# Optimization experiments

Hardware: AMD Instinct MI355X
Metric: run time of the kernel (lower is better)

Reference implementation:

```python
import jax, jax.numpy as jnp
import numpy as np

HID = 2048; H = 16; QLR = 1536; KVLR = 512
DN = 128   # qk_nope_head_dim
DR = 64    # qk_rope_head_dim
DV = 128   # v_head_dim
EPS = 1e-6
B, S = 2, 2048


def rmsnorm(x):
    return x * jax.lax.rsqrt(jnp.mean(x * x, axis=-1, keepdims=True) + EPS)


def rope_tables(seq_len):
    inv_freq = 1.0 / (10000.0 ** (jnp.arange(0, DR, 2, dtype=jnp.float32) / DR))  # [DR/2]
    ang = jnp.arange(seq_len, dtype=jnp.float32)[:, None] * inv_freq[None, :]     # [S, DR/2]
    cos = jnp.concatenate([jnp.cos(ang), jnp.cos(ang)], axis=-1)                  # [S, DR]
    sin = jnp.concatenate([jnp.sin(ang), jnp.sin(ang)], axis=-1)
    return cos, sin


def apply_rope(x, cos, sin):
    # x: [B, h, S, DR]; half-split rotation
    half = DR // 2
    rh = jnp.concatenate([-x[..., half:], x[..., :half]], axis=-1)
    return x * cos + rh * sin


def setup_inputs() -> dict:
    key = jax.random.key(0)
    ks = jax.random.split(key, 7)
    w = 0.02
    inp = {
        "X": jax.random.normal(ks[0], (B, S, HID), dtype=jnp.float32),
        "attention_mask": jnp.tril(jnp.ones((S, S), dtype=jnp.int32)),
        "Wq_down": jax.random.normal(ks[1], (HID, QLR), dtype=jnp.float32) * w,
        "bq_down": jnp.zeros((QLR,), dtype=jnp.float32),
        "Wq_up": jax.random.normal(ks[2], (QLR, H * (DN + DR)), dtype=jnp.float32) * w,
        "bq_up": jnp.zeros((H * (DN + DR),), dtype=jnp.float32),
        "Wkv_down": jax.random.normal(ks[3], (HID, DR + KVLR), dtype=jnp.float32) * w,
        "bkv_down": jnp.zeros((DR + KVLR,), dtype=jnp.float32),
        "Wkv_up": jax.random.normal(ks[4], (KVLR, H * (DN + DV)), dtype=jnp.float32) * w,
        "bkv_up": jnp.zeros((H * (DN + DV),), dtype=jnp.float32),
        "Wo": jax.random.normal(ks[5], (H * DV, HID), dtype=jnp.float32) * w,
        "bo": jnp.zeros((HID,), dtype=jnp.float32),
    }
    return inp


def reference(X, attention_mask, Wq_down, bq_down, Wq_up, bq_up,
              Wkv_down, bkv_down, Wkv_up, bkv_up, Wo, bo):
    b, s, _ = X.shape
    # query path: low-rank down -> RMSNorm -> up
    q = rmsnorm(X @ Wq_down + bq_down) @ Wq_up + bq_up            # [B,S,H*(DN+DR)]
    q = q.reshape(b, s, H, DN + DR).transpose(0, 2, 1, 3)          # [B,H,S,DN+DR]
    q_nope, q_rope = q[..., :DN], q[..., DN:]
    # kv path: shared rope key + compressed latent
    ckv = X @ Wkv_down + bkv_down                                  # [B,S,DR+KVLR]
    k_rope = ckv[..., :DR].reshape(b, s, 1, DR).transpose(0, 2, 1, 3)  # [B,1,S,DR]
    kv = rmsnorm(ckv[..., DR:]) @ Wkv_up + bkv_up                  # [B,S,H*(DN+DV)]
    kv = kv.reshape(b, s, H, DN + DV).transpose(0, 2, 1, 3)        # [B,H,S,DN+DV]
    k_nope, value = kv[..., :DN], kv[..., DN:]
    # decoupled RoPE
    cos, sin = rope_tables(s)
    q_rope = apply_rope(q_rope, cos, sin)
    k_rope = apply_rope(k_rope, cos, sin)
    query = jnp.concatenate([q_nope, q_rope], axis=-1)             # [B,H,S,DN+DR]
    key = jnp.concatenate([k_nope, jnp.broadcast_to(k_rope, (b, H, s, DR))], axis=-1)
    # attention (manual matmul -> mask -> softmax -> matmul; dropout p=0)
    scale = 1.0 / np.sqrt(DN + DR)
    scores = jnp.einsum('bhqd,bhkd->bhqk', query, key) * scale     # [B,H,S,S]
    scores = jnp.where(attention_mask[None, None, :, :] == 0, -jnp.inf, scores)
    probs = jax.nn.softmax(scores, axis=-1)
    attn = jnp.einsum('bhqk,bhkd->bhqd', probs, value)             # [B,H,S,DV]
    attn = attn.transpose(0, 2, 1, 3).reshape(b, s, H * DV)
    return attn @ Wo + bo
```

## Files before the change

kernel.cpp:

```cpp
#include <hip/hip_runtime.h>

#define HID 2048
#define NH 16
#define QLR 1536
#define KVLR 512
#define DN 128
#define DR 64
#define DV 128
#define BB 2
#define SS 2048
#define NTOK (BB*SS)
#define QD 3072
#define KVD 4096
#define CKVD 576
#define NQT2 (SS/128)

typedef __bf16 bf16x8 __attribute__((ext_vector_type(8)));
typedef float f32x4 __attribute__((ext_vector_type(4)));
typedef float f32x16 __attribute__((ext_vector_type(16)));
typedef unsigned short us4v __attribute__((ext_vector_type(4)));
typedef unsigned int u32x4 __attribute__((ext_vector_type(4)));

__device__ __forceinline__ unsigned short f2bf(float f){
  unsigned u = __builtin_bit_cast(unsigned, f);
  return (unsigned short)((u + 0x7fffu + ((u>>16)&1u)) >> 16);
}
__device__ __forceinline__ float bf2f(unsigned short h){
  unsigned u = ((unsigned)h)<<16; return __builtin_bit_cast(float, u);
}
__device__ __forceinline__ unsigned cvt_pk_bf16(float a, float b){
  unsigned r;
  asm("v_cvt_pk_bf16_f32 %0, %1, %2" : "=v"(r) : "v"(a), "v"(b));
  return r;
}

#define GLOAD16(g, l) __builtin_amdgcn_global_load_lds( \
    (const __attribute__((address_space(1))) void*)(const void*)(g), \
    (__attribute__((address_space(3))) void*)(void*)(l), 16, 0, 0)

__global__ void cvt_f32_bf16(const float* __restrict__ in, unsigned short* __restrict__ out, int n4){
  int i = blockIdx.x*256 + threadIdx.x;
  if (i < n4){
    float4 v = ((const float4*)in)[i];
    us4v o = { f2bf(v.x), f2bf(v.y), f2bf(v.z), f2bf(v.w) };
    ((us4v*)out)[i] = o;
  }
}

__global__ void wtrans(const float* __restrict__ W, unsigned short* __restrict__ WT,
                       int K, int N){
  __shared__ float t[32][33];
  int n0 = blockIdx.x*32, k0 = blockIdx.y*32;
  int tx = threadIdx.x & 31, ty = threadIdx.x >> 5;
  #pragma unroll
  for (int i = ty; i < 32; i += 8){
    int k = k0 + i, n = n0 + tx;
    t[i][tx] = (n < N) ? W[(size_t)k*N + n] : 0.f;
  }
  __syncthreads();
  #pragma unroll
  for (int i = ty; i < 32; i += 8){
    int n = n0 + i, k = k0 + tx;
    WT[(size_t)n*K + k] = f2bf(t[tx][i]);
  }
}

template<bool OUTF32>
__device__ __forceinline__ void gemm_core(
  unsigned short* As, unsigned short* Bs,
  const unsigned short* __restrict__ A, int lda,
  const unsigned short* __restrict__ BT,
  const float* __restrict__ bias,
  void* __restrict__ Cv, int ldc,
  int N, int K, int bx, int by)
{
  const int tid = threadIdx.x;
  const int wave = tid>>6, lane = tid&63, lq = lane&15, lg = lane>>4;
  const int tm = by*128, tn = bx*128;
  const int wm = (wave>>1)*64, wn = (wave&1)*64;
  f32x4 acc[4][4] = {};
  char* AsB = (char*)As; char* BsB = (char*)Bs;
  const int r8 = tid>>3;
  const int sc = ((tid&7) ^ (r8&7))*8;
  for (int kt = 0; kt < K; kt += 64){
    __syncthreads();
    #pragma unroll
    for (int rd=0; rd<4; rd++){
      GLOAD16(A  + (size_t)(tm + rd*32 + r8)*lda + kt + sc, AsB + rd*4096 + wave*1024);
      GLOAD16(BT + (size_t)(tn + rd*32 + r8)*K   + kt + sc, BsB + rd*4096 + wave*1024);
    }
    asm volatile("s_waitcnt vmcnt(0)" ::: "memory");
    __syncthreads();
    #pragma unroll
    for (int h=0; h<2; h++){
      bf16x8 af[4], bfr[4];
      #pragma unroll
      for (int i=0;i<4;i++) af[i]  = *(const bf16x8*)(AsB + (wm+16*i+lq)*128 + ((((h*4+lg)^(lq&7)))<<4));
      #pragma unroll
      for (int j=0;j<4;j++) bfr[j] = *(const bf16x8*)(BsB + (wn+16*j+lq)*128 + ((((h*4+lg)^(lq&7)))<<4));
      #pragma unroll
      for (int i=0;i<4;i++)
        #pragma unroll
        for (int j=0;j<4;j++)
          acc[i][j] = __builtin_amdgcn_mfma_f32_16x16x32_bf16(af[i], bfr[j], acc[i][j], 0,0,0);
    }
  }
  #pragma unroll
  for (int i=0;i<4;i++){
    #pragma unroll
    for (int j=0;j<4;j++){
      int col = tn + wn + 16*j + lq;
      if (col < N){
        float bv = bias ? bias[col] : 0.f;
        #pragma unroll
        for (int r=0;r<4;r++){
          int row = tm + wm + 16*i + lg*4 + r;
          float v = acc[i][j][r] + bv;
          if (OUTF32) ((float*)Cv)[(size_t)row*ldc + col] = v;
          else ((unsigned short*)Cv)[(size_t)row*ldc + col] = f2bf(v);
        }
      }
    }
  }
}

__device__ __forceinline__ void xcd_remap(int& bx, int& by){
  int nwg = gridDim.x*gridDim.y;
  int lin = blockIdx.y*gridDim.x + blockIdx.x;
  int wg = (lin&7)*(nwg>>3) + (lin>>3);
  bx = wg % gridDim.x; by = wg / gridDim.x;
}

template<bool OUTF32>
__global__ __launch_bounds__(256) void gemm_bt(
  const unsigned short* __restrict__ A, int lda,
  const unsigned short* __restrict__ BT,
  const float* __restrict__ bias,
  void* __restrict__ Cv, int ldc, int N, int K)
{
  __shared__ unsigned short As[128*64];
  __shared__ unsigned short Bs[128*64];
  int bx, by; xcd_remap(bx, by);
  gemm_core<OUTF32>(As, Bs, A, lda, BT, bias, Cv, ldc, N, K, bx, by);
}

__global__ __launch_bounds__(256) void gemm_bt_dual(
  const unsigned short* __restrict__ A0, int lda0, const unsigned short* __restrict__ BT0,
  const float* __restrict__ b0, void* __restrict__ C0, int ldc0, int N0, int K0,
  const unsigned short* __restrict__ A1, int lda1, const unsigned short* __restrict__ BT1,
  const float* __restrict__ b1, void* __restrict__ C1, int ldc1, int N1, int K1,
  int split)
{
  __shared__ unsigned short As[128*64];
  __shared__ unsigned short Bs[128*64];
  int bx, by; xcd_remap(bx, by);
  if (bx < split)
    gemm_core<false>(As, Bs, A0, lda0, BT0, b0, C0, ldc0, N0, K0, bx, by);
  else
    gemm_core<false>(As, Bs, A1, lda1, BT1, b1, C1, ldc1, N1, K1, bx - split, by);
}

__device__ __forceinline__ void rms_row(unsigned short* x, int D, float* red){
  int tid = threadIdx.x;
  float ss = 0.f;
  for (int i = tid; i < D; i += 256){ float v = bf2f(x[i]); ss += v*v; }
  #pragma unroll
  for (int o=32;o;o>>=1) ss += __shfl_xor(ss, o, 64);
  if ((tid&63)==0) red[tid>>6] = ss;
  __syncthreads();
  float tot = red[0]+red[1]+red[2]+red[3];
  float sc = rsqrtf(tot/(float)D + 1e-6f);
  for (int i = tid; i < D; i += 256) x[i] = f2bf(bf2f(x[i])*sc);
}

__global__ void norms_fused(unsigned short* __restrict__ cq,
                            unsigned short* __restrict__ ckv,
                            unsigned short* __restrict__ kr){
  __shared__ float red[4];
  int bid = blockIdx.x;
  if (bid < NTOK){
    rms_row(cq + (size_t)bid*QLR, QLR, red);
  } else if (bid < 2*NTOK){
    rms_row(ckv + (size_t)(bid-NTOK)*CKVD + DR, KVLR, red);
  } else {
    int idx = (bid - 2*NTOK)*256 + threadIdx.x;
    int j = idx & 31;
    int t = idx >> 5;
    int s = t & (SS-1);
    const unsigned short* src = ckv + (size_t)t*CKVD;
    float xr = bf2f(src[j]), xi = bf2f(src[j+32]);
    float freq = powf(10000.f, -(float)(2*j)/64.f);
    float ang = (float)s * freq;
    float c = cosf(ang), sn = sinf(ang);
    kr[(size_t)t*64 + j]      = f2bf(xr*c - xi*sn);
    kr[(size_t)t*64 + j + 32] = f2bf(xi*c + xr*sn);
  }
}

__global__ void ropeq_vt_fused(unsigned short* __restrict__ q,
                               const unsigned short* __restrict__ kv,
                               unsigned short* __restrict__ vT){
  int bid = blockIdx.x;
  if (bid < NTOK*NH*32/256){
    int idx = bid*256 + threadIdx.x;
    int j = idx & 31;
    int h = (idx >> 5) & 15;
    int t = idx >> 9;
    int s = t & (SS-1);
    unsigned short* base = q + (size_t)t*QD + h*(DN+DR) + DN;
    float xr = bf2f(base[j]), xi = bf2f(base[j+32]);
    float freq = powf(10000.f, -(float)(2*j)/64.f);
    float ang = (float)s * freq;
    float c = cosf(ang), sn = sinf(ang);
    base[j]    = f2bf(xr*c - xi*sn);
    base[j+32] = f2bf(xi*c + xr*sn);
  } else {
    __shared__ unsigned short t[32][33];
    int idx = bid - NTOK*NH*32/256;
    int s0 = (idx & 63)*32, d0 = ((idx>>6)&3)*32, bh = idx>>8;
    int b = bh>>4, h = bh&15;
    int tx = threadIdx.x & 31, ty = threadIdx.x >> 5;
    #pragma unroll
    for (int i = ty; i < 32; i += 8)
      t[i][tx] = kv[((size_t)(b*SS + s0+i))*KVD + h*(DN+DV) + DN + d0 + tx];
    __syncthreads();
    #pragma unroll
    for (int i = ty; i < 32; i += 8)
      vT[((size_t)(bh*DV + d0+i))*SS + s0 + tx] = t[tx][i];
  }
}

__global__ __launch_bounds__(256) void attn_kernel(
  const unsigned short* __restrict__ q,
  const unsigned short* __restrict__ kv,
  const unsigned short* __restrict__ kr,
  const unsigned short* __restrict__ vT,
  unsigned short* __restrict__ attn)
{
  __shared__ unsigned short Ksn[2][32*128];
  __shared__ unsigned short Ksr[2][32*64];
  __shared__ unsigned short Vs [2][128*32];
  __shared__ unsigned short Ps [4*32*36];
  const int tid = threadIdx.x, wave = tid>>6, lane = tid&63;
  const int lo = lane&31, hi = lane>>5;
  const int lin = blockIdx.x;
  const int bh = (lin&7) + 8*((lin>>3)&3);
  const int qt = NQT2-1 - (lin>>5);
  const int b = bh>>4, h = bh&15;
  const float kmul = 1.44269504f * 0.07216878364f;

  const int rK = tid>>4, cK = (tid&15) ^ (rK&7);
  const int rR = tid>>3, cR = (tid&7) ^ (rR&7);
  const int rV = tid>>2, cV = (tid&3) ^ (rV&3);
  const unsigned short* pKn0 = kv + (size_t)(b*SS + rK)*KVD + h*(DN+DV) + cK*8;
  const unsigned short* pKn1 = pKn0 + (size_t)16*KVD;
  const unsigned short* pKr  = kr + (size_t)(b*SS + rR)*64 + cR*8;
  const unsigned short* pV0  = vT + ((size_t)bh*DV + rV)*SS + cV*8;
  const unsigned short* pV1  = pV0 + (size_t)64*SS;

#define STAGE_ATTN(bufi) do {                                                 \
    GLOAD16(pKn0, (char*)Ksn[bufi] +        wave*1024);                       \
    GLOAD16(pKn1, (char*)Ksn[bufi] + 4096 + wave*1024);                       \
    GLOAD16(pKr,  (char*)Ksr[bufi] +        wave*1024);                       \
    GLOAD16(pV0,  (char*)Vs[bufi]  +        wave*1024);                       \
    GLOAD16(pV1,  (char*)Vs[bufi]  + 4096 + wave*1024);                       \
    pKn0 += 32*KVD; pKn1 += 32*KVD; pKr += 32*64; pV0 += 32; pV1 += 32;       \
  } while(0)

  const int qw = qt*128 + wave*32;
  const int myq = qw + lo;
  bf16x8 qf[12];
  {
    const unsigned short* qrow = q + (size_t)(b*SS + myq)*QD + h*(DN+DR);
    #pragma unroll
    for (int c=0;c<12;c++) qf[c] = *(const bf16x8*)(qrow + c*16 + hi*8);
  }
  f32x16 oacc[4] = {};
  float m = -1e30f, lsum = 0.f;
  const int nkt = 4*qt + 4;

  STAGE_ATTN(0);
  asm volatile("s_waitcnt vmcnt(0)" ::: "memory");
  __builtin_amdgcn_s_barrier();
  int cur = 0;
  for (int kt = 0; kt < nkt; kt++){
    if (kt+1 < nkt) STAGE_ATTN(cur^1);
    f32x16 sacc = {};
    __builtin_amdgcn_s_setprio(1);
    #pragma unroll
    for (int ck=0;ck<8;ck++){
      bf16x8 kf = *(const bf16x8*)((char*)Ksn[cur] + lo*256 + ((((ck*2+hi)^(lo&7)))<<4));
      sacc = __builtin_amdgcn_mfma_f32_32x32x16_bf16(kf, qf[ck], sacc, 0,0,0);
    }
    #pragma unroll
    for (int ck=0;ck<4;ck++){
      bf16x8 kf = *(const bf16x8*)((char*)Ksr[cur] + lo*128 + ((((ck*2+hi)^(lo&7)))<<4));
      sacc = __builtin_amdgcn_mfma_f32_32x32x16_bf16(kf, qf[8+ck], sacc, 0,0,0);
    }
    __builtin_amdgcn_s_setprio(0);
    float s[16]; float pmax = -1e30f;
    if (kt*32 + 31 <= qw){
      #pragma unroll
      for (int r=0;r<16;r++){ float v = sacc[r]*kmul; s[r]=v; pmax=fmaxf(pmax,v); }
    } else {
      #pragma unroll
      for (int r=0;r<16;r++){
        int kpos = kt*32 + (r&3) + 8*(r>>2) + 4*hi;
        float v = (kpos <= myq) ? sacc[r]*kmul : -1e30f;
        s[r]=v; pmax=fmaxf(pmax,v);
      }
    }
    pmax = fmaxf(pmax, __shfl_xor(pmax, 32, 64));
    if (!__all(pmax <= m + 8.f)){
      float mnew = fmaxf(m, pmax);
      float alpha = __builtin_amdgcn_exp2f(m - mnew);
      m = mnew; lsum *= alpha;
      #pragma unroll
      for (int dt=0;dt<4;dt++)
        #pragma unroll
        for (int r=0;r<16;r++) oacc[dt][r] *= alpha;
    }
    float psum = 0.f;
    #pragma unroll
    for (int r=0;r<16;r++){ s[r] = __builtin_amdgcn_exp2f(s[r] - m); psum += s[r]; }
    psum += __shfl_xor(psum, 32, 64);
    lsum += psum;
    unsigned short* Pw = Ps + wave*32*36;
    #pragma unroll
    for (int rg=0; rg<4; rg++){
      uint2 pk = { cvt_pk_bf16(s[rg*4+0], s[rg*4+1]),
                   cvt_pk_bf16(s[rg*4+2], s[rg*4+3]) };
      *(uint2*)((char*)Pw + lo*72 + rg*16 + hi*8) = pk;
    }
    bf16x8 pf[2];
    #pragma unroll
    for (int j=0;j<2;j++){
      uint2 a0 = *(const uint2*)((char*)Pw + lo*72 + (2*j+hi)*16);
      uint2 a1 = *(const uint2*)((char*)Pw + lo*72 + (2*j+hi)*16 + 8);
      u32x4 pk4 = { a0.x, a0.y, a1.x, a1.y };
      pf[j] = __builtin_bit_cast(bf16x8, pk4);
    }
    __builtin_amdgcn_s_setprio(1);
    #pragma unroll
    for (int dt=0; dt<4; dt++){
      const int row = dt*32 + lo;
      #pragma unroll
      for (int j=0;j<2;j++){
        bf16x8 vf = *(const bf16x8*)((char*)Vs[cur] + row*64 + ((((j*2+hi)^(lo&3)))<<4));
        oacc[dt] = __builtin_amdgcn_mfma_f32_32x32x16_bf16(vf, pf[j], oacc[dt], 0,0,0);
      }
    }
    __builtin_amdgcn_s_setprio(0);
    asm volatile("s_waitcnt vmcnt(0)" ::: "memory");
    __builtin_amdgcn_s_barrier();
    cur ^= 1;
  }
  float inv = 1.f / lsum;
  unsigned short* orow = attn + (size_t)(b*SS + myq)*2048 + h*DV;
  #pragma unroll
  for (int dt=0; dt<4; dt++){
    #pragma unroll
    for (int rq=0; rq<4; rq++){
      int dbase = dt*32 + rq*8 + hi*4;
      uint2 o = { cvt_pk_bf16(oacc[dt][rq*4+0]*inv, oacc[dt][rq*4+1]*inv),
                  cvt_pk_bf16(oacc[dt][rq*4+2]*inv, oacc[dt][rq*4+3]*inv) };
      *(uint2*)(orow + dbase) = o;
    }
  }
#undef STAGE_ATTN
}

extern "C" void kernel_launch(void* const* d_in, const int* in_sizes, int n_in,
                              void* d_out, int out_size, void* d_ws, size_t ws_size,
                              hipStream_t stream){
  const float* X    = (const float*)d_in[0];
  const float* Wqd  = (const float*)d_in[2];
  const float* bqd  = (const float*)d_in[3];
  const float* Wqu  = (const float*)d_in[4];
  const float* bqu  = (const float*)d_in[5];
  const float* Wkvd = (const float*)d_in[6];
  const float* bkvd = (const float*)d_in[7];
  const float* Wkvu = (const float*)d_in[8];
  const float* bkvu = (const float*)d_in[9];
  const float* Wo   = (const float*)d_in[10];
  const float* bo   = (const float*)d_in[11];
  float* out = (float*)d_out;

  char* ws = (char*)d_ws;
  unsigned short* Xb    = (unsigned short*)(ws + 0);
  unsigned short* attnb = (unsigned short*)(ws + 0);
  char*           arena = ws + 16777216;
  unsigned short* Wt1 = (unsigned short*)(arena);
  unsigned short* Wt3 = (unsigned short*)(arena + 6291456);
  unsigned short* Wt2 = (unsigned short*)(arena);
  unsigned short* Wt4 = (unsigned short*)(arena + 9437184);
  unsigned short* Wt5 = (unsigned short*)(arena);
  unsigned short* cq   = (unsigned short*)(ws + 31457280);
  unsigned short* qtmp = (unsigned short*)(ws + 44040192);
  unsigned short* ckv  = (unsigned short*)(ws + 69206016);
  unsigned short* kvt  = (unsigned short*)(ws + 73924608);
  unsigned short* kr   = (unsigned short*)(ws + 107479040);
  unsigned short* vT   = (unsigned short*)(ws + 108003328);

  cvt_f32_bf16<<<dim3(NTOK*HID/4/256), 256, 0, stream>>>(X, Xb, NTOK*HID/4);
  wtrans<<<dim3(QLR/32, HID/32), 256, 0, stream>>>(Wqd, Wt1, HID, QLR);
  wtrans<<<dim3(640/32, HID/32), 256, 0, stream>>>(Wkvd, Wt3, HID, CKVD);
  gemm_bt_dual<<<dim3(QLR/128 + 640/128, NTOK/128), 256, 0, stream>>>(
      Xb, HID, Wt1, bqd, cq, QLR, QLR, HID,
      Xb, HID, Wt3, bkvd, ckv, CKVD, CKVD, HID, QLR/128);
  norms_fused<<<dim3(2*NTOK + NTOK*32/256), 256, 0, stream>>>(cq, ckv, kr);
  wtrans<<<dim3(QD/32, QLR/32), 256, 0, stream>>>(Wqu, Wt2, QLR, QD);
  wtrans<<<dim3(KVD/32, KVLR/32), 256, 0, stream>>>(Wkvu, Wt4, KVLR, KVD);
  gemm_bt_dual<<<dim3(QD/128 + KVD/128, NTOK/128), 256, 0, stream>>>(
      cq, QLR, Wt2, bqu, qtmp, QD, QD, QLR,
      ckv + DR, CKVD, Wt4, bkvu, kvt, KVD, KVD, KVLR, QD/128);
  ropeq_vt_fused<<<dim3(NTOK*NH*32/256 + 8192), 256, 0, stream>>>(qtmp, kvt, vT);
  attn_kernel<<<dim3(NQT2 * BB*NH), 256, 0, stream>>>(qtmp, kvt, kr, vT, attnb);
  wtrans<<<dim3(HID/32, HID/32), 256, 0, stream>>>(Wo, Wt5, HID, HID);
  gemm_bt<true><<<dim3(HID/128, NTOK/128), 256, 0, stream>>>(attnb, HID, Wt5, bo, out, HID, HID, HID);
}
```

Before: 361.1 us.

## Split long causal attention query tiles across two KV segments and combine

The twelve largest query tiles per head now have their KV range split into two halves, each handled by its own block. Each block writes a normalized partial output plus its running max and sum to workspace. A new combine kernel merges each pair with log-sum-exp weights. This is meant to balance the causal workload across blocks and shorten the tail, at the cost of an extra launch, partial-output traffic and extra bf16 rounding of the partial results.

```diff
diff --git a/kernel.cpp b/kernel.cpp
--- a/kernel.cpp
+++ b/kernel.cpp
@@ -235,7 +235,10 @@
   const unsigned short* __restrict__ kv,
   const unsigned short* __restrict__ kr,
   const unsigned short* __restrict__ vT,
-  unsigned short* __restrict__ attn)
+  unsigned short* __restrict__ attn,
+  unsigned short* __restrict__ OpA,
+  unsigned short* __restrict__ OpC,
+  float2* __restrict__ mlp)
 {
   __shared__ unsigned short Ksn[2][32*128];
   __shared__ unsigned short Ksr[2][32*64];
@@ -245,17 +248,29 @@
   const int lo = lane&31, hi = lane>>5;
   const int lin = blockIdx.x;
   const int bh = (lin&7) + 8*((lin>>3)&3);
-  const int qt = NQT2-1 - (lin>>5);
+  const int rest = lin>>5;
+  int qt, k0, nseg, pidx = 0;
+  if (rest < 24){
+    qt = 15 - (rest>>1);
+    int seg = rest & 1;
+    nseg = 2*qt + 2;
+    k0 = seg ? nseg : 0;
+    pidx = ((rest>>1)*32 + bh)*2 + seg;
+  } else {
+    qt = 27 - rest;
+    nseg = 4*qt + 4;
+    k0 = 0;
+  }
   const int b = bh>>4, h = bh&15;
   const float kmul = 1.44269504f * 0.07216878364f;
 
   const int rK = tid>>4, cK = (tid&15) ^ (rK&7);
   const int rR = tid>>3, cR = (tid&7) ^ (rR&7);
   const int rV = tid>>2, cV = (tid&3) ^ (rV&3);
-  const unsigned short* pKn0 = kv + (size_t)(b*SS + rK)*KVD + h*(DN+DV) + cK*8;
+  const unsigned short* pKn0 = kv + (size_t)(b*SS + k0*32 + rK)*KVD + h*(DN+DV) + cK*8;
   const unsigned short* pKn1 = pKn0 + (size_t)16*KVD;
-  const unsigned short* pKr  = kr + (size_t)(b*SS + rR)*64 + cR*8;
-  const unsigned short* pV0  = vT + ((size_t)bh*DV + rV)*SS + cV*8;
+  const unsigned short* pKr  = kr + (size_t)(b*SS + k0*32 + rR)*64 + cR*8;
+  const unsigned short* pV0  = vT + ((size_t)bh*DV + rV)*SS + k0*32 + cV*8;
   const unsigned short* pV1  = pV0 + (size_t)64*SS;
 
 #define STAGE_ATTN(bufi) do {                                                 \
@@ -277,14 +292,14 @@
   }
   f32x16 oacc[4] = {};
   float m = -1e30f, lsum = 0.f;
-  const int nkt = 4*qt + 4;
+  const int kend = k0 + nseg;
 
   STAGE_ATTN(0);
   asm volatile("s_waitcnt vmcnt(0)" ::: "memory");
   __builtin_amdgcn_s_barrier();
   int cur = 0;
-  for (int kt = 0; kt < nkt; kt++){
-    if (kt+1 < nkt) STAGE_ATTN(cur^1);
+  for (int kt = k0; kt < kend; kt++){
+    if (kt+1 < kend) STAGE_ATTN(cur^1);
     f32x16 sacc = {};
     __builtin_amdgcn_s_setprio(1);
     #pragma unroll
@@ -356,18 +371,71 @@
     cur ^= 1;
   }
   float inv = 1.f / lsum;
-  unsigned short* orow = attn + (size_t)(b*SS + myq)*2048 + h*DV;
+  if (rest < 24){
+    unsigned short* Op = (pidx < 448) ? OpA + (size_t)pidx*16384
+                                      : OpC + (size_t)(pidx-448)*16384;
+    const int prow = wave*32 + lo;
+    #pragma unroll
+    for (int dt=0; dt<4; dt++){
+      #pragma unroll
+      for (int rq=0; rq<4; rq++){
+        int dbase = dt*32 + rq*8 + hi*4;
+        uint2 o = { cvt_pk_bf16(oacc[dt][rq*4+0]*inv, oacc[dt][rq*4+1]*inv),
+                    cvt_pk_bf16(oacc[dt][rq*4+2]*inv, oacc[dt][rq*4+3]*inv) };
+        *(uint2*)(Op + prow*128 + dbase) = o;
+      }
+    }
+    if (hi == 0) mlp[(size_t)pidx*128 + prow] = make_float2(m, lsum);
+  } else {
+    unsigned short* orow = attn + (size_t)(b*SS + myq)*2048 + h*DV;
+    #pragma unroll
+    for (int dt=0; dt<4; dt++){
+      #pragma unroll
+      for (int rq=0; rq<4; rq++){
+        int dbase = dt*32 + rq*8 + hi*4;
+        uint2 o = { cvt_pk_bf16(oacc[dt][rq*4+0]*inv, oacc[dt][rq*4+1]*inv),
+                    cvt_pk_bf16(oacc[dt][rq*4+2]*inv, oacc[dt][rq*4+3]*inv) };
+        *(uint2*)(orow + dbase) = o;
+      }
+    }
+  }
+#undef STAGE_ATTN
+}
+
+__global__ __launch_bounds__(256) void attn_combine(
+  const unsigned short* __restrict__ OpA, const unsigned short* __restrict__ OpC,
+  const float2* __restrict__ mlp, unsigned short* __restrict__ attn)
+{
+  int pair = blockIdx.x;
+  int qt = 15 - (pair >> 5);
+  int bh = pair & 31;
+  int b = bh>>4, h = bh&15;
+  int t = threadIdx.x;
+  int row = t >> 1, dh = (t&1)*64;
+  int p0 = pair*2, p1 = pair*2 + 1;
+  const unsigned short* O0 = ((p0 < 448) ? OpA + (size_t)p0*16384 : OpC + (size_t)(p0-448)*16384) + row*128 + dh;
+  const unsigned short* O1 = ((p1 < 448) ? OpA + (size_t)p1*16384 : OpC + (size_t)(p1-448)*16384) + row*128 + dh;
+  float2 a = mlp[(size_t)p0*128 + row];
+  float2 c = mlp[(size_t)p1*128 + row];
+  float M = fmaxf(a.x, c.x);
+  float w0 = a.y * __builtin_amdgcn_exp2f(a.x - M);
+  float w1 = c.y * __builtin_amdgcn_exp2f(c.x - M);
+  float inv = 1.f / (w0 + w1);
+  w0 *= inv; w1 *= inv;
+  unsigned short* dst = attn + (size_t)(b*SS + qt*128 + row)*2048 + h*DV + dh;
   #pragma unroll
-  for (int dt=0; dt<4; dt++){
-    #pragma unroll
-    for (int rq=0; rq<4; rq++){
-      int dbase = dt*32 + rq*8 + hi*4;
-      uint2 o = { cvt_pk_bf16(oacc[dt][rq*4+0]*inv, oacc[dt][rq*4+1]*inv),
-                  cvt_pk_bf16(oacc[dt][rq*4+2]*inv, oacc[dt][rq*4+3]*inv) };
-      *(uint2*)(orow + dbase) = o;
-    }
-  }
-#undef STAGE_ATTN
+  for (int i = 0; i < 64; i += 8){
+    u32x4 v0 = *(const u32x4*)(O0 + i);
+    u32x4 v1 = *(const u32x4*)(O1 + i);
+    const unsigned short* s0 = (const unsigned short*)&v0;
+    const unsigned short* s1 = (const unsigned short*)&v1;
+    float f[8];
+    #pragma unroll
+    for (int j=0;j<8;j++) f[j] = bf2f(s0[j])*w0 + bf2f(s1[j])*w1;
+    u32x4 o = { cvt_pk_bf16(f[0],f[1]), cvt_pk_bf16(f[2],f[3]),
+                cvt_pk_bf16(f[4],f[5]), cvt_pk_bf16(f[6],f[7]) };
+    *(u32x4*)(dst + i) = o;
+  }
 }
 
 extern "C" void kernel_launch(void* const* d_in, const int* in_sizes, int n_in,
@@ -401,6 +469,9 @@
   unsigned short* kvt  = (unsigned short*)(ws + 73924608);
   unsigned short* kr   = (unsigned short*)(ws + 107479040);
   unsigned short* vT   = (unsigned short*)(ws + 108003328);
+  unsigned short* OpA  = (unsigned short*)(arena);
+  unsigned short* OpC  = (unsigned short*)(ws + 31457280);
+  float2*         mlp  = (float2*)(ws + 69206016);
 
   cvt_f32_bf16<<<dim3(NTOK*HID/4/256), 256, 0, stream>>>(X, Xb, NTOK*HID/4);
   wtrans<<<dim3(QLR/32, HID/32), 256, 0, stream>>>(Wqd, Wt1, HID, QLR);
@@ -415,7 +486,8 @@
       cq, QLR, Wt2, bqu, qtmp, QD, QD, QLR,
       ckv + DR, CKVD, Wt4, bkvu, kvt, KVD, KVD, KVLR, QD/128);
   ropeq_vt_fused<<<dim3(NTOK*NH*32/256 + 8192), 256, 0, stream>>>(qtmp, kvt, vT);
-  attn_kernel<<<dim3(NQT2 * BB*NH), 256, 0, stream>>>(qtmp, kvt, kr, vT, attnb);
+  attn_kernel<<<dim3(896), 256, 0, stream>>>(qtmp, kvt, kr, vT, attnb, OpA, OpC, mlp);
+  attn_combine<<<dim3(384), 256, 0, stream>>>(OpA, OpC, mlp, attnb);
   wtrans<<<dim3(HID/32, HID/32), 256, 0, stream>>>(Wo, Wt5, HID, HID);
   gemm_bt<true><<<dim3(HID/128, NTOK/128), 256, 0, stream>>>(attnb, HID, Wt5, bo, out, HID, HID, HID);
 }
```

Measured after the change: 403.7 us. +11.8%, slower.

## Triple-buffer GEMM shared-memory tiles with async global loads over K=32 stages

Applied to the files above, without the earlier changes.

Rewrites the GEMM main loop from a single-buffered K=64 tile into a three-stage ring of K=32 tiles. Global-to-LDS loads for stage t+2 are issued before computing stage t, with partial vmcnt waits. This is meant to hide global memory latency behind MFMA work and cut the number of full barriers per tile. In exchange it uses a new swizzle pattern for 64-byte rows and 1.5x the LDS, and it issues more loop iterations with less MFMA work per barrier.

```diff
diff --git a/kernel.cpp b/kernel.cpp
--- a/kernel.cpp
+++ b/kernel.cpp
@@ -80,31 +80,50 @@
   const int wm = (wave>>1)*64, wn = (wave&1)*64;
   f32x4 acc[4][4] = {};
   char* AsB = (char*)As; char* BsB = (char*)Bs;
-  const int r8 = tid>>3;
-  const int sc = ((tid&7) ^ (r8&7))*8;
-  for (int kt = 0; kt < K; kt += 64){
-    __syncthreads();
-    #pragma unroll
-    for (int rd=0; rd<4; rd++){
-      GLOAD16(A  + (size_t)(tm + rd*32 + r8)*lda + kt + sc, AsB + rd*4096 + wave*1024);
-      GLOAD16(BT + (size_t)(tn + rd*32 + r8)*K   + kt + sc, BsB + rd*4096 + wave*1024);
-    }
-    asm volatile("s_waitcnt vmcnt(0)" ::: "memory");
-    __syncthreads();
-    #pragma unroll
-    for (int h=0; h<2; h++){
-      bf16x8 af[4], bfr[4];
+  const int r4 = tid>>2;
+  const int rowS0 = r4, rowS1 = 64 + r4;
+  const int c0 = ((tid&3) ^ ((rowS0 ^ (rowS0>>2)) & 3))*8;
+  const int c1 = ((tid&3) ^ ((rowS1 ^ (rowS1>>2)) & 3))*8;
+  const unsigned short* Arow0 = A  + (size_t)(tm + rowS0)*lda + c0;
+  const unsigned short* Arow1 = A  + (size_t)(tm + rowS1)*lda + c1;
+  const unsigned short* Brow0 = BT + (size_t)(tn + rowS0)*K   + c0;
+  const unsigned short* Brow1 = BT + (size_t)(tn + rowS1)*K   + c1;
+  const int nt = K >> 5;
+
+#define GSTAGE(t_) do { const int bq_ = ((t_)%3)*8192; const int kk_ = (t_)*32; \
+    GLOAD16(Arow0 + kk_, AsB + bq_ +        tid*16);                            \
+    GLOAD16(Arow1 + kk_, AsB + bq_ + 4096 + tid*16);                            \
+    GLOAD16(Brow0 + kk_, BsB + bq_ +        tid*16);                            \
+    GLOAD16(Brow1 + kk_, BsB + bq_ + 4096 + tid*16); } while(0)
+
+  GSTAGE(0); GSTAGE(1);
+  asm volatile("s_waitcnt vmcnt(4)" ::: "memory");
+  __builtin_amdgcn_s_barrier();
+  for (int t = 0; t < nt; t++){
+    const int cur = t%3;
+    if (t+2 < nt) GSTAGE(t+2);
+    bf16x8 af[4], bfr[4];
+    #pragma unroll
+    for (int i=0;i<4;i++){
+      int row = wm+16*i+lq;
+      af[i]  = *(const bf16x8*)(AsB + cur*8192 + row*64 + ((lg ^ ((row ^ (row>>2))&3))<<4));
+    }
+    #pragma unroll
+    for (int j=0;j<4;j++){
+      int row = wn+16*j+lq;
+      bfr[j] = *(const bf16x8*)(BsB + cur*8192 + row*64 + ((lg ^ ((row ^ (row>>2))&3))<<4));
+    }
+    #pragma unroll
+    for (int i=0;i<4;i++)
       #pragma unroll
-      for (int i=0;i<4;i++) af[i]  = *(const bf16x8*)(AsB + (wm+16*i+lq)*128 + ((((h*4+lg)^(lq&7)))<<4));
-      #pragma unroll
-      for (int j=0;j<4;j++) bfr[j] = *(const bf16x8*)(BsB + (wn+16*j+lq)*128 + ((((h*4+lg)^(lq&7)))<<4));
-      #pragma unroll
-      for (int i=0;i<4;i++)
-        #pragma unroll
-        for (int j=0;j<4;j++)
-          acc[i][j] = __builtin_amdgcn_mfma_f32_16x16x32_bf16(af[i], bfr[j], acc[i][j], 0,0,0);
-    }
-  }
+      for (int j=0;j<4;j++)
+        acc[i][j] = __builtin_amdgcn_mfma_f32_16x16x32_bf16(af[i], bfr[j], acc[i][j], 0,0,0);
+    if (t+2 < nt) asm volatile("s_waitcnt vmcnt(4)" ::: "memory");
+    else          asm volatile("s_waitcnt vmcnt(0)" ::: "memory");
+    __builtin_amdgcn_s_barrier();
+  }
+#undef GSTAGE
+
   #pragma unroll
   for (int i=0;i<4;i++){
     #pragma unroll
@@ -138,8 +157,8 @@
   const float* __restrict__ bias,
   void* __restrict__ Cv, int ldc, int N, int K)
 {
-  __shared__ unsigned short As[128*64];
-  __shared__ unsigned short Bs[128*64];
+  __shared__ unsigned short As[3*128*32];
+  __shared__ unsigned short Bs[3*128*32];
   int bx, by; xcd_remap(bx, by);
   gemm_core<OUTF32>(As, Bs, A, lda, BT, bias, Cv, ldc, N, K, bx, by);
 }
@@ -151,8 +170,8 @@
   const float* __restrict__ b1, void* __restrict__ C1, int ldc1, int N1, int K1,
   int split)
 {
-  __shared__ unsigned short As[128*64];
-  __shared__ unsigned short Bs[128*64];
+  __shared__ unsigned short As[3*128*32];
+  __shared__ unsigned short Bs[3*128*32];
   int bx, by; xcd_remap(bx, by);
   if (bx < split)
     gemm_core<false>(As, Bs, A0, lda0, BT0, b0, C0, ldc0, N0, K0, bx, by);
```

Measured after the change: 390.2 us. 1.08x slower.
